# Optimization experiments

Measured on AMD Instinct MI355X. Metric: run time of the kernel, lower is better.

## Reference

```python
import jax, jax.numpy as jnp
import numpy as np

B, R, A, L, P = 1024, 512, 196, 2, 4  # batch, rnn_size, att_size, num_layers, num_parallels


def setup_inputs() -> dict:
    key = jax.random.key(0)
    ks = jax.random.split(key, 24)
    s = 0.02
    inp = {
        'x': jax.random.normal(ks[0], (B, R), jnp.float32),
        'att': jax.random.normal(ks[1], (B, A, R), jnp.float32),
        'inputs': jax.random.normal(ks[2], (2 * L, B, R), jnp.float32),
        # first attention block
        'Wa2a': jax.random.normal(ks[3], (A, R), jnp.float32) * s,
        'ba2a': jnp.zeros((A,), jnp.float32),
        'Wh2a': jax.random.normal(ks[4], (A, R), jnp.float32) * s,
        'bh2a': jnp.zeros((A,), jnp.float32),
        'Wd2d': jax.random.normal(ks[5], (1, A), jnp.float32) * s,
        'bd2d': jnp.zeros((1,), jnp.float32),
        # second attention block
        'Wa2a1': jax.random.normal(ks[6], (A, R), jnp.float32) * s,
        'ba2a1': jnp.zeros((A,), jnp.float32),
        'Wh2a1': jax.random.normal(ks[7], (A, R), jnp.float32) * s,
        'bh2a1': jnp.zeros((A,), jnp.float32),
        'Wd2d1': jax.random.normal(ks[8], (1, A), jnp.float32) * s,
        'bd2d1': jnp.zeros((1,), jnp.float32),
        # per-parallel LSTM gate linears, stacked over P
        'Wi2h': jax.random.normal(ks[9], (P, 4 * R, R), jnp.float32) * s,
        'bi2h': jnp.zeros((P, 4 * R), jnp.float32),
        'Wh2h': jax.random.normal(ks[10], (P, 4 * R, R), jnp.float32) * s,
        'bh2h': jnp.zeros((P, 4 * R), jnp.float32),
        'Wa2h': jax.random.normal(ks[11], (P, 4 * R, R), jnp.float32) * s,
        'ba2h': jnp.zeros((P, 4 * R), jnp.float32),
    }
    return inp


def _attend(att, h, Wa, ba, Wh, bh, Wd, bd):
    # att: [B, S, R] with S == A (code requires it); h: [B, R]
    av = jnp.einsum('bsr,ar->bsa', att, Wa) + ba            # [B, S, A]
    ah = h @ Wh.T + bh                                      # [B, A]
    # original expands h-projection along the LAST axis (unsqueeze(2).expand)
    dot = jnp.tanh(av + ah[:, :, None])                     # [B, S, A]
    score = jnp.einsum('bsa,a->bs', dot, Wd[0]) + bd[0]     # [B, S]
    w = jax.nn.softmax(score, axis=-1)
    return jnp.einsum('bsr,bs->br', att, w)                 # [B, R]


def reference(x, att, inputs, Wa2a, ba2a, Wh2a, bh2a, Wd2d, bd2d,
              Wa2a1, ba2a1, Wh2a1, bh2a1, Wd2d1, bd2d1,
              Wi2h, bi2h, Wh2h, bh2h, Wa2h, ba2h):
    R_ = x.shape[-1]
    L_ = inputs.shape[0] // 2
    outputs = []
    for i in range(L_):
        prev_c = inputs[2 * i]
        prev_h = inputs[2 * i + 1]
        xt = x if i == 0 else x + outputs[-1]
        att_res = _attend(att, prev_h, Wa2a, ba2a, Wh2a, bh2a, Wd2d, bd2d)
        # stacked per-parallel gate sums: [P, B, 4R]
        sums = (jnp.einsum('bd,pgd->pbg', xt, Wi2h) + bi2h[:, None, :]
                + jnp.einsum('bd,pgd->pbg', prev_h, Wh2h) + bh2h[:, None, :]
                + jnp.einsum('bd,pgd->pbg', att_res, Wa2h) + ba2h[:, None, :])
        ig = jax.nn.sigmoid(sums[..., :R_])
        fg = jax.nn.sigmoid(sums[..., R_:2 * R_])
        og = jax.nn.sigmoid(sums[..., 2 * R_:3 * R_])
        it = jnp.tanh(sums[..., 3 * R_:])
        nc = fg * prev_c[None] + ig * it                    # [P, B, R]
        next_c = nc.mean(axis=0)
        next_h = (og * jnp.tanh(nc)).mean(axis=0)
        att_res1 = _attend(att, next_h, Wa2a1, ba2a1, Wh2a1, bh2a1, Wd2d1, bd2d1)
        top_h = att_res1 + next_h
        outputs.append(next_c)
        outputs.append(top_h)
    return jnp.stack(outputs)  # [2L, B, R]
```

## Files before the change

### kernel.cpp

```cpp
#include <hip/hip_runtime.h>
#include <math.h>

typedef __attribute__((ext_vector_type(8))) unsigned short ushort8_t;
typedef __attribute__((ext_vector_type(8))) short bf16x8;
typedef __attribute__((ext_vector_type(4))) float f32x4;

namespace {

constexpr int Bn = 1024;
constexpr int Rn = 512;
constexpr int An = 196;
constexpr int Gn = 8192;
constexpr int Kcat = 1536;
constexpr int NP = 224;
constexpr long ROWS = (long)Bn * An;

__device__ __forceinline__ float b2f(unsigned short u) {
  union { unsigned int i; float f; } v; v.i = ((unsigned int)u) << 16; return v.f;
}
__device__ __forceinline__ unsigned short f2b(float f) {
  union { float f; unsigned int i; } v; v.f = f;
  unsigned int r = v.i + 0x7fffu + ((v.i >> 16) & 1u);
  return (unsigned short)(r >> 16);
}
__device__ __forceinline__ float sigmf(float x) {
  return __builtin_amdgcn_rcpf(1.f + __expf(-x));
}
__device__ __forceinline__ float tanhf_fast(float x) {
  const float e = __expf(2.f * x);
  return 1.f - 2.f * __builtin_amdgcn_rcpf(e + 1.f);
}

__global__ __launch_bounds__(256)
void f2b_copy(const float* __restrict__ src, unsigned short* __restrict__ dst, long n)
{
  long i = ((long)blockIdx.x * 256 + threadIdx.x) * 8;
  const long stride = (long)gridDim.x * 256 * 8;
  for (; i + 8 <= n; i += stride) {
    float4 a = *(const float4*)(src + i);
    float4 b = *(const float4*)(src + i + 4);
    ushort8_t o;
    o[0] = f2b(a.x); o[1] = f2b(a.y); o[2] = f2b(a.z); o[3] = f2b(a.w);
    o[4] = f2b(b.x); o[5] = f2b(b.y); o[6] = f2b(b.z); o[7] = f2b(b.w);
    *(ushort8_t*)(dst + i) = o;
  }
}

__global__ __launch_bounds__(256)
void pack_all(const float* __restrict__ Wa0, const float* __restrict__ Wa1,
              const float* __restrict__ Wh0, const float* __restrict__ Wh1,
              const float* __restrict__ inputs, const float* __restrict__ x,
              const float* __restrict__ Wi, const float* __restrict__ Wh,
              const float* __restrict__ Wa,
              unsigned short* __restrict__ Wp, unsigned short* __restrict__ whcat,
              unsigned short* __restrict__ h01,
              unsigned short* __restrict__ X20, unsigned short* __restrict__ X21,
              unsigned short* __restrict__ W2)
{
  const int blk = blockIdx.x;
  if (blk < 112) {
    long i = ((long)blk * 256 + threadIdx.x) * 8;
    if (i >= 2L * NP * 512) return;
    const int set = (int)(i / (NP * 512));
    const int rem = (int)(i % (NP * 512));
    const int row = rem / 512, k = rem % 512;
    ushort8_t o;
    if (row < An) {
      const float* s = (set ? Wa1 : Wa0) + (long)row * 512 + k;
      float4 a = *(const float4*)s, b = *(const float4*)(s + 4);
      o[0] = f2b(a.x); o[1] = f2b(a.y); o[2] = f2b(a.z); o[3] = f2b(a.w);
      o[4] = f2b(b.x); o[5] = f2b(b.y); o[6] = f2b(b.z); o[7] = f2b(b.w);
    } else {
      o = ushort8_t{0,0,0,0,0,0,0,0};
    }
    *(ushort8_t*)(Wp + i) = o;
  } else if (blk < 210) {
    long i = ((long)(blk - 112) * 256 + threadIdx.x) * 8;
    if (i >= 2L * An * 512) return;
    const long half = (long)An * 512;
    const float* s = (i < half) ? Wh0 + i : Wh1 + (i - half);
    float4 v0 = *(const float4*)s, v1 = *(const float4*)(s + 4);
    ushort8_t o;
    o[0] = f2b(v0.x); o[1] = f2b(v0.y); o[2] = f2b(v0.z); o[3] = f2b(v0.w);
    o[4] = f2b(v1.x); o[5] = f2b(v1.y); o[6] = f2b(v1.z); o[7] = f2b(v1.w);
    *(ushort8_t*)(whcat + i) = o;
  } else if (blk < 722) {
    long i = ((long)(blk - 210) * 256 + threadIdx.x) * 8;
    if (i >= 2L * Bn * 512) return;
    const long half = (long)Bn * 512;
    const float* s = (i < half) ? inputs + half + i : inputs + 3 * half + (i - half);
    float4 v0 = *(const float4*)s, v1 = *(const float4*)(s + 4);
    ushort8_t o;
    o[0] = f2b(v0.x); o[1] = f2b(v0.y); o[2] = f2b(v0.z); o[3] = f2b(v0.w);
    o[4] = f2b(v1.x); o[5] = f2b(v1.y); o[6] = f2b(v1.z); o[7] = f2b(v1.w);
    *(ushort8_t*)(h01 + i) = o;
  } else if (blk < 1490) {
    long i = ((long)(blk - 722) * 256 + threadIdx.x) * 8;
    if (i >= 3L * Bn * 512) return;
    const int sec = (int)(i / ((long)Bn * 512));
    const long r = i % ((long)Bn * 512);
    const int b = (int)(r >> 9);
    const int k = (int)(r & 511);
    const float* src = (sec == 0 ? x
                     : sec == 1 ? inputs + (long)Bn * Rn
                     : inputs + 3L * Bn * Rn) + r;
    unsigned short* dst = (sec == 2 ? X21 : X20) + (long)b * Kcat + (sec ? 512 : 0) + k;
    float4 v0 = *(const float4*)src, v1 = *(const float4*)(src + 4);
    ushort8_t o;
    o[0] = f2b(v0.x); o[1] = f2b(v0.y); o[2] = f2b(v0.z); o[3] = f2b(v0.w);
    o[4] = f2b(v1.x); o[5] = f2b(v1.y); o[6] = f2b(v1.z); o[7] = f2b(v1.w);
    *(ushort8_t*)dst = o;
  } else {
    long i = ((long)(blk - 1490) * 256 + threadIdx.x) * 8;
    if (i >= (long)Gn * Kcat) return;
    const int g = (int)(i / Kcat);
    const int k = (int)(i % Kcat);
    const float* src = (k < 512) ? Wi + (long)g * 512 + k
                     : (k < 1024) ? Wh + (long)g * 512 + (k - 512)
                     : Wa + (long)g * 512 + (k - 1024);
    float4 a = *(const float4*)src;
    float4 b = *(const float4*)(src + 4);
    ushort8_t o;
    o[0] = f2b(a.x); o[1] = f2b(a.y); o[2] = f2b(a.z); o[3] = f2b(a.w);
    o[4] = f2b(b.x); o[5] = f2b(b.y); o[6] = f2b(b.z); o[7] = f2b(b.w);
    *(ushort8_t*)(W2 + i) = o;
  }
}

__global__ __launch_bounds__(512, 4)
void av_cs(const unsigned short* __restrict__ A,
           const unsigned short* __restrict__ Wpad,
           const float* __restrict__ b0vec, const float* __restrict__ b1vec,
           const float* __restrict__ Wd,
           const float* __restrict__ ah0, const float* __restrict__ ah1,
           float* __restrict__ s0, float* __restrict__ s1,
           unsigned short* __restrict__ av_out)
{
  __shared__ unsigned short As[128 * 32];
  __shared__ unsigned short Bs[224 * 32];
  __shared__ float wds[NP], bas[NP];
  __shared__ float ahAs[128], ahBs[128];
  __shared__ float sbA[128], sbB[128];

  const int tid = threadIdx.x;
  const int lane = tid & 63, w = tid >> 6;
  const int wr = w >> 1, wc = w & 1;
  const int fr = lane & 15, q = lane >> 4;
  const int d = blockIdx.x;
  const int xt = ((d >> 4) << 3) | (d & 7);
  const int set = (d >> 3) & 1;
  const long row0 = (long)xt * 128;

  if (set == 0) {
    if (tid < NP) {
      wds[tid] = (tid < An) ? Wd[tid] : 0.f;
      bas[tid] = (tid < An) ? b0vec[tid] : 0.f;
    }
    if (tid >= 256 && tid < 384) ahAs[tid - 256] = ah0[row0 + tid - 256];
    if (tid >= 384)              ahBs[tid - 384] = ah1[row0 + tid - 384];
  } else {
    if (tid < NP) bas[tid] = (tid < An) ? b1vec[tid] : 0.f;
  }

  const unsigned short* Ab = A + row0 * 512;
  const unsigned short* Bb = Wpad + (long)set * NP * 512;

  f32x4 acc[2][7] = {};

  const int grow = lane >> 2;
  const int gchk = (lane & 3) * 8;

  for (int kt = 0; kt < 512; kt += 32) {
    {
      const unsigned short* src = Ab + (long)(w * 16 + grow) * 512 + gchk + kt;
      __builtin_amdgcn_global_load_lds(
          (const __attribute__((address_space(1))) unsigned int*)src,
          (__attribute__((address_space(3))) unsigned int*)(As + w * 512), 16, 0, 0);
    }
    {
      const unsigned short* src = Bb + (long)(w * 16 + grow) * 512 + gchk + kt;
      __builtin_amdgcn_global_load_lds(
          (const __attribute__((address_space(1))) unsigned int*)src,
          (__attribute__((address_space(3))) unsigned int*)(Bs + w * 512), 16, 0, 0);
    }
    if (w < 6) {
      const unsigned short* src = Bb + (long)((w + 8) * 16 + grow) * 512 + gchk + kt;
      __builtin_amdgcn_global_load_lds(
          (const __attribute__((address_space(1))) unsigned int*)src,
          (__attribute__((address_space(3))) unsigned int*)(Bs + (w + 8) * 512), 16, 0, 0);
    }
    __syncthreads();
    bf16x8 af[2], bfr[7];
#pragma unroll
    for (int m = 0; m < 2; ++m)
      af[m] = *(const bf16x8*)&As[(wr * 32 + m * 16 + fr) * 32 + q * 8];
#pragma unroll
    for (int n = 0; n < 7; ++n)
      bfr[n] = *(const bf16x8*)&Bs[(wc * 112 + n * 16 + fr) * 32 + q * 8];
#pragma unroll
    for (int m = 0; m < 2; ++m)
#pragma unroll
      for (int n = 0; n < 7; ++n)
        acc[m][n] = __builtin_amdgcn_mfma_f32_16x16x32_bf16(af[m], bfr[n], acc[m][n], 0, 0, 0);
    __syncthreads();
  }

  if (set == 0) {
    float pA[2][4], pB[2][4];
#pragma unroll
    for (int m = 0; m < 2; ++m)
#pragma unroll
      for (int j = 0; j < 4; ++j) { pA[m][j] = 0.f; pB[m][j] = 0.f; }
#pragma unroll
    for (int n = 0; n < 7; ++n) {
      const int col = wc * 112 + n * 16 + fr;
      const float wd = wds[col];
      const float bv = bas[col];
#pragma unroll
      for (int m = 0; m < 2; ++m) {
#pragma unroll
        for (int j = 0; j < 4; ++j) {
          const int rl = wr * 32 + m * 16 + q * 4 + j;
          const float av = acc[m][n][j] + bv;
          pA[m][j] += wd * tanhf_fast(av + ahAs[rl]);
          pB[m][j] += wd * tanhf_fast(av + ahBs[rl]);
        }
      }
    }
#pragma unroll
    for (int m = 0; m < 2; ++m)
#pragma unroll
      for (int j = 0; j < 4; ++j) {
#pragma unroll
        for (int off = 1; off < 16; off <<= 1) {
          pA[m][j] += __shfl_xor(pA[m][j], off);
          pB[m][j] += __shfl_xor(pB[m][j], off);
        }
      }
    __syncthreads();
    if (wc == 0 && fr == 0) {
#pragma unroll
      for (int m = 0; m < 2; ++m)
#pragma unroll
        for (int j = 0; j < 4; ++j) {
          const int rl = wr * 32 + m * 16 + q * 4 + j;
          sbA[rl] = pA[m][j]; sbB[rl] = pB[m][j];
        }
    }
    __syncthreads();
    if (wc == 1 && fr == 0) {
#pragma unroll
      for (int m = 0; m < 2; ++m)
#pragma unroll
        for (int j = 0; j < 4; ++j) {
          const int rl = wr * 32 + m * 16 + q * 4 + j;
          sbA[rl] += pA[m][j]; sbB[rl] += pB[m][j];
        }
    }
    __syncthreads();
    if (tid < 128) {
      s0[row0 + tid] = sbA[tid];
      s1[row0 + tid] = sbB[tid];
    }
  } else {
#pragma unroll
    for (int n = 0; n < 7; ++n) {
      const int col = wc * 112 + n * 16 + fr;
      if (col >= An) continue;
      const float bv = bas[col];
#pragma unroll
      for (int m = 0; m < 2; ++m) {
#pragma unroll
        for (int j = 0; j < 4; ++j) {
          const long row = row0 + wr * 32 + m * 16 + q * 4 + j;
          av_out[row * An + col] = f2b(acc[m][n][j] + bv);
        }
      }
    }
  }
}

__global__ __launch_bounds__(256)
void gemm_gate(const unsigned short* __restrict__ A, const unsigned short* __restrict__ Bm,
               const float* __restrict__ b1, const float* __restrict__ b2,
               const float* __restrict__ b3, float* __restrict__ C)
{
  __shared__ unsigned short As[128 * 32];
  __shared__ unsigned short Bs[128 * 32];
  const int tid = threadIdx.x;
  const int lane = tid & 63, w = tid >> 6;
  int bid = blockIdx.x;
  bid = (bid & 7) * (gridDim.x >> 3) + (bid >> 3);
  const int bx = bid & 63;
  const int by = bid >> 6;
  const long row0 = (long)by * 128;
  const long col0 = (long)bx * 128;
  const int wr = w >> 1, wc = w & 1;
  const int fr = lane & 15, q = lane >> 4;
  const int srow = lane >> 2, schk = lane & 3;

  f32x4 acc[4][4] = {};
  const unsigned short* A0 = A + row0 * Kcat + schk * 8;
  const unsigned short* B0 = Bm + col0 * Kcat + schk * 8;

  for (int kt = 0; kt < Kcat; kt += 32) {
#pragma unroll
    for (int i = 0; i < 2; ++i) {
      const int rr = (w * 2 + i) * 16 + srow;
      __builtin_amdgcn_global_load_lds(
          (const __attribute__((address_space(1))) unsigned int*)(A0 + (long)rr * Kcat + kt),
          (__attribute__((address_space(3))) unsigned int*)(As + (w * 2 + i) * 512),
          16, 0, 0);
      __builtin_amdgcn_global_load_lds(
          (const __attribute__((address_space(1))) unsigned int*)(B0 + (long)rr * Kcat + kt),
          (__attribute__((address_space(3))) unsigned int*)(Bs + (w * 2 + i) * 512),
          16, 0, 0);
    }
    __syncthreads();
    bf16x8 af[4], bfr[4];
#pragma unroll
    for (int m = 0; m < 4; ++m)
      af[m] = *(const bf16x8*)&As[(wr * 64 + m * 16 + fr) * 32 + q * 8];
#pragma unroll
    for (int n = 0; n < 4; ++n)
      bfr[n] = *(const bf16x8*)&Bs[(wc * 64 + n * 16 + fr) * 32 + q * 8];
#pragma unroll
    for (int m = 0; m < 4; ++m)
#pragma unroll
      for (int n = 0; n < 4; ++n)
        acc[m][n] = __builtin_amdgcn_mfma_f32_16x16x32_bf16(af[m], bfr[n], acc[m][n], 0, 0, 0);
    __syncthreads();
  }

  const int crow = wr * 64 + q * 4;
  const int ccol = wc * 64 + fr;
#pragma unroll
  for (int n = 0; n < 4; ++n) {
    const int col = (int)col0 + ccol + n * 16;
    const float bv = b1[col] + b2[col] + b3[col];
#pragma unroll
    for (int m = 0; m < 4; ++m) {
      const long rb = row0 + crow + m * 16;
#pragma unroll
      for (int j = 0; j < 4; ++j)
        C[(rb + j) * (long)Gn + col] = acc[m][n][j] + bv;
    }
  }
}

__global__ __launch_bounds__(256)
void gemm_bf(const unsigned short* __restrict__ A, const unsigned short* __restrict__ Bm,
             const float* __restrict__ bias, float* __restrict__ C,
             int N, int K, int ldc)
{
  constexpr int LDP = 56;
  __shared__ unsigned short As[128 * LDP];
  __shared__ unsigned short Bs[128 * LDP];
  const int tid = threadIdx.x;
  const long row0 = (long)blockIdx.y * 128;
  const int col0 = blockIdx.x * 128;
  const int wid = tid >> 6, lane = tid & 63;
  const int wr = wid >> 1, wc = wid & 1;
  const int fr = lane & 15, kg = (lane >> 4) * 8;

  f32x4 acc[4][4] = {};

  const int srow = tid >> 1;
  const int skh = tid & 1;
  const unsigned short* Ap = A + (row0 + srow) * (long)K + skh * 16;
  const int bcol = col0 + srow;
  const unsigned short* Bp = Bm + (long)(bcol < N ? bcol : N - 1) * K + skh * 16;

  ushort8_t a0 = *(const ushort8_t*)(Ap);
  ushort8_t a1 = *(const ushort8_t*)(Ap + 8);
  ushort8_t b0 = *(const ushort8_t*)(Bp);
  ushort8_t b1 = *(const ushort8_t*)(Bp + 8);

  const int sw = srow * LDP + skh * 16;
  for (int kt = 0; kt < K; kt += 32) {
    *(ushort8_t*)&As[sw] = a0;
    *(ushort8_t*)&As[sw + 8] = a1;
    *(ushort8_t*)&Bs[sw] = b0;
    *(ushort8_t*)&Bs[sw + 8] = b1;
    if (kt + 32 < K) {
      a0 = *(const ushort8_t*)(Ap + kt + 32);
      a1 = *(const ushort8_t*)(Ap + kt + 40);
      b0 = *(const ushort8_t*)(Bp + kt + 32);
      b1 = *(const ushort8_t*)(Bp + kt + 40);
    }
    __syncthreads();
    bf16x8 af[4], bfr[4];
#pragma unroll
    for (int m = 0; m < 4; ++m)
      af[m] = *(const bf16x8*)&As[(wr * 64 + m * 16 + fr) * LDP + kg];
#pragma unroll
    for (int n = 0; n < 4; ++n)
      bfr[n] = *(const bf16x8*)&Bs[(wc * 64 + n * 16 + fr) * LDP + kg];
#pragma unroll
    for (int m = 0; m < 4; ++m)
#pragma unroll
      for (int n = 0; n < 4; ++n)
        acc[m][n] = __builtin_amdgcn_mfma_f32_16x16x32_bf16(af[m], bfr[n], acc[m][n], 0, 0, 0);
    __syncthreads();
  }

  const int crow = wr * 64 + (lane >> 4) * 4;
  const int ccol = wc * 64 + fr;
#pragma unroll
  for (int n = 0; n < 4; ++n) {
    const int col = col0 + ccol + n * 16;
    if (col >= N) continue;
    const float bv = bias ? bias[col] : 0.f;
#pragma unroll
    for (int m = 0; m < 4; ++m) {
      const long rb = row0 + crow + m * 16;
#pragma unroll
      for (int j = 0; j < 4; ++j)
        C[(rb + j) * (long)ldc + col] = acc[m][n][j] + bv;
    }
  }
}

__global__ __launch_bounds__(256)
void score1(const unsigned short* __restrict__ av, const float* __restrict__ ah,
            const float* __restrict__ Wd, float* __restrict__ s0)
{
  const int row = blockIdx.x * 4 + (threadIdx.x >> 6);
  const int lane = threadIdx.x & 63;
  const float A0 = ah[row];
  float v0 = 0.f;
  if (lane < 49) {
    ushort4 u = *(const ushort4*)(av + (long)row * An + lane * 4);
    float4 w = *(const float4*)(Wd + lane * 4);
    v0 = w.x * tanhf_fast(b2f(u.x) + A0) + w.y * tanhf_fast(b2f(u.y) + A0)
       + w.z * tanhf_fast(b2f(u.z) + A0) + w.w * tanhf_fast(b2f(u.w) + A0);
  }
#pragma unroll
  for (int o = 32; o; o >>= 1) v0 += __shfl_down(v0, o);
  if (lane == 0) s0[row] = v0;
}

__global__ __launch_bounds__(256)
void wsumA(const unsigned short* __restrict__ att,
           const float* __restrict__ scA, const float* __restrict__ scB,
           unsigned short* __restrict__ X20, unsigned short* __restrict__ X21)
{
  const int half = threadIdx.x >> 7;
  const int b = blockIdx.x * 2 + half;
  const int t = threadIdx.x & 127;
  const int wv = t >> 6;
  __shared__ float ws0[2][An], ws1[2][An];
  __shared__ float redm[2][2][2], redsum[2][2][2];

  const float r0a = scA[(long)b * An + t];
  const float r0b = (t + 128 < An) ? scA[(long)b * An + t + 128] : -3.0e38f;
  const float r1a = scB[(long)b * An + t];
  const float r1b = (t + 128 < An) ? scB[(long)b * An + t + 128] : -3.0e38f;
  float m0 = fmaxf(r0a, r0b), m1 = fmaxf(r1a, r1b);
#pragma unroll
  for (int o = 32; o; o >>= 1) {
    m0 = fmaxf(m0, __shfl_xor(m0, o));
    m1 = fmaxf(m1, __shfl_xor(m1, o));
  }
  if ((t & 63) == 0) { redm[0][half][wv] = m0; redm[1][half][wv] = m1; }
  __syncthreads();
  m0 = fmaxf(redm[0][half][0], redm[0][half][1]);
  m1 = fmaxf(redm[1][half][0], redm[1][half][1]);
  const float e0a = __expf(r0a - m0);
  const float e0b = (t + 128 < An) ? __expf(r0b - m0) : 0.f;
  const float e1a = __expf(r1a - m1);
  const float e1b = (t + 128 < An) ? __expf(r1b - m1) : 0.f;
  float sl0 = e0a + e0b, sl1 = e1a + e1b;
#pragma unroll
  for (int o = 32; o; o >>= 1) {
    sl0 += __shfl_xor(sl0, o);
    sl1 += __shfl_xor(sl1, o);
  }
  if ((t & 63) == 0) { redsum[0][half][wv] = sl0; redsum[1][half][wv] = sl1; }
  __syncthreads();
  const float inv0 = __builtin_amdgcn_rcpf(redsum[0][half][0] + redsum[0][half][1]);
  const float inv1 = __builtin_amdgcn_rcpf(redsum[1][half][0] + redsum[1][half][1]);
  ws0[half][t] = e0a * inv0;
  ws1[half][t] = e1a * inv1;
  if (t + 128 < An) {
    ws0[half][t + 128] = e0b * inv0;
    ws1[half][t + 128] = e1b * inv1;
  }
  __syncthreads();

  const unsigned short* ap = att + (long)b * An * Rn + t * 4;
  float a00 = 0, a01 = 0, a02 = 0, a03 = 0;
  float a10 = 0, a11 = 0, a12 = 0, a13 = 0;
  for (int s = 0; s < An; ++s) {
    ushort4 u = *(const ushort4*)(ap + (long)s * Rn);
    const float f0 = b2f(u.x), f1 = b2f(u.y), f2 = b2f(u.z), f3 = b2f(u.w);
    const float v0 = ws0[half][s];
    a00 = fmaf(f0, v0, a00); a01 = fmaf(f1, v0, a01);
    a02 = fmaf(f2, v0, a02); a03 = fmaf(f3, v0, a03);
    const float v1 = ws1[half][s];
    a10 = fmaf(f0, v1, a10); a11 = fmaf(f1, v1, a11);
    a12 = fmaf(f2, v1, a12); a13 = fmaf(f3, v1, a13);
  }
  const long base = (long)b * Kcat + 1024 + t * 4;
  ushort4 oA, oB;
  oA.x = f2b(a00); oA.y = f2b(a01); oA.z = f2b(a02); oA.w = f2b(a03);
  oB.x = f2b(a10); oB.y = f2b(a11); oB.z = f2b(a12); oB.w = f2b(a13);
  *(ushort4*)(X20 + base) = oA;
  *(ushort4*)(X21 + base) = oB;
}

template<bool WX2>
__global__ __launch_bounds__(256)
void wsumB(const unsigned short* __restrict__ att,
           const float* __restrict__ sc, const float* __restrict__ nh,
           const float* __restrict__ xin,
           float* __restrict__ outp, unsigned short* __restrict__ X21)
{
  const int half = threadIdx.x >> 7;
  const int b = blockIdx.x * 2 + half;
  const int t = threadIdx.x & 127;
  const int wv = t >> 6;
  __shared__ float ws[2][An];
  __shared__ float redm[2][2], redsum[2][2];

  const float ra = sc[(long)b * An + t];
  const float rb = (t + 128 < An) ? sc[(long)b * An + t + 128] : -3.0e38f;
  float m0 = fmaxf(ra, rb);
#pragma unroll
  for (int o = 32; o; o >>= 1) m0 = fmaxf(m0, __shfl_xor(m0, o));
  if ((t & 63) == 0) redm[half][wv] = m0;
  __syncthreads();
  m0 = fmaxf(redm[half][0], redm[half][1]);
  const float ea = __expf(ra - m0);
  const float eb = (t + 128 < An) ? __expf(rb - m0) : 0.f;
  float sl = ea + eb;
#pragma unroll
  for (int o = 32; o; o >>= 1) sl += __shfl_xor(sl, o);
  if ((t & 63) == 0) redsum[half][wv] = sl;
  __syncthreads();
  const float inv = __builtin_amdgcn_rcpf(redsum[half][0] + redsum[half][1]);
  ws[half][t] = ea * inv;
  if (t + 128 < An) ws[half][t + 128] = eb * inv;
  __syncthreads();

  const unsigned short* ap = att + (long)b * An * Rn + t * 4;
  float a0 = 0, a1 = 0, a2 = 0, a3 = 0;
  for (int s = 0; s < An; ++s) {
    ushort4 u = *(const ushort4*)(ap + (long)s * Rn);
    const float w = ws[half][s];
    a0 = fmaf(b2f(u.x), w, a0); a1 = fmaf(b2f(u.y), w, a1);
    a2 = fmaf(b2f(u.z), w, a2); a3 = fmaf(b2f(u.w), w, a3);
  }
  const long base = (long)b * Rn + t * 4;
  float4 ad = *(const float4*)(nh + base);
  a0 += ad.x; a1 += ad.y; a2 += ad.z; a3 += ad.w;
  *(float4*)(outp + base) = make_float4(a0, a1, a2, a3);
  if (WX2) {
    float4 xv = *(const float4*)(xin + base);
    ushort4 o;
    o.x = f2b(a0 + xv.x); o.y = f2b(a1 + xv.y);
    o.z = f2b(a2 + xv.z); o.w = f2b(a3 + xv.w);
    *(ushort4*)(X21 + (long)b * Kcat + t * 4) = o;
  }
}

__global__ __launch_bounds__(256)
void gates_pw(const float* __restrict__ sums, const float* __restrict__ prev_c,
              float* __restrict__ out_c, float* __restrict__ nh,
              unsigned short* __restrict__ nh_bf)
{
  const int i = blockIdx.x * 256 + threadIdx.x;
  const int b = i >> 9;
  const int r = i & 511;
  const float c = prev_c[i];
  float aC = 0.f, aH = 0.f;
#pragma unroll
  for (int p = 0; p < 4; ++p) {
    const float* sp = sums + (long)b * Gn + p * 2048 + r;
    const float ig = sigmf(sp[0]);
    const float fg = sigmf(sp[512]);
    const float og = sigmf(sp[1024]);
    const float it = tanhf_fast(sp[1536]);
    const float nc = fmaf(fg, c, ig * it);
    aC += nc;
    aH = fmaf(og, tanhf_fast(nc), aH);
  }
  out_c[i] = aC * 0.25f;
  const float hv = aH * 0.25f;
  nh[i] = hv;
  nh_bf[i] = f2b(hv);
}

}

extern "C" void kernel_launch(void* const* d_in, const int* in_sizes, int n_in,
                              void* d_out, int out_size, void* d_ws, size_t ws_size,
                              hipStream_t stream)
{
  const float* x      = (const float*)d_in[0];
  const float* att    = (const float*)d_in[1];
  const float* inputs = (const float*)d_in[2];
  const float* Wa2a   = (const float*)d_in[3];
  const float* ba2a   = (const float*)d_in[4];
  const float* Wh2a   = (const float*)d_in[5];
  const float* bh2a   = (const float*)d_in[6];
  const float* Wd2d   = (const float*)d_in[7];
  const float* Wa2a1  = (const float*)d_in[9];
  const float* ba2a1  = (const float*)d_in[10];
  const float* Wh2a1  = (const float*)d_in[11];
  const float* bh2a1  = (const float*)d_in[12];
  const float* Wd2d1  = (const float*)d_in[13];
  const float* Wi2h   = (const float*)d_in[15];
  const float* bi2h   = (const float*)d_in[16];
  const float* Wh2h   = (const float*)d_in[17];
  const float* bh2h   = (const float*)d_in[18];
  const float* Wa2h   = (const float*)d_in[19];
  const float* ba2h   = (const float*)d_in[20];
  (void)in_sizes; (void)n_in; (void)out_size; (void)ws_size;

  float* out = (float*)d_out;
  const float* prev_c0 = inputs + 0 * (long)Bn * Rn;
  const float* prev_c1 = inputs + 2 * (long)Bn * Rn;

  char* wsp = (char*)d_ws;
  size_t off = 0;
  auto alloc = [&](size_t bytes) -> void* {
    void* p = wsp + off;
    off += (bytes + 1023) & ~(size_t)1023;
    return p;
  };
  unsigned short* att_bf  = (unsigned short*)alloc(ROWS * Rn * 2);
  unsigned short* W2      = (unsigned short*)alloc((size_t)Gn * Kcat * 2);
  unsigned short* Wpad    = (unsigned short*)alloc((size_t)2 * NP * Rn * 2);
  unsigned short* whcat   = (unsigned short*)alloc((size_t)2 * An * Rn * 2);
  unsigned short* h01_bf  = (unsigned short*)alloc((size_t)2 * Bn * Rn * 2);
  unsigned short* nh_bf   = (unsigned short*)alloc((size_t)Bn * Rn * 2);
  unsigned short* X20     = (unsigned short*)alloc((size_t)Bn * Kcat * 2);
  unsigned short* X21     = (unsigned short*)alloc((size_t)Bn * Kcat * 2);
  unsigned short* av1_bf  = (unsigned short*)alloc(ROWS * An * 2);
  float* ahAB = (float*)alloc((size_t)2 * ROWS * 4);
  float* ah1  = (float*)alloc(ROWS * 4);
  float* scA  = (float*)alloc(ROWS * 4);
  float* scB  = (float*)alloc(ROWS * 4);
  float* sc1  = (float*)alloc(ROWS * 4);
  float* nh   = (float*)alloc((size_t)Bn * Rn * 4);
  float* sums = (float*)alloc((size_t)Bn * Gn * 4);

  float* ahA = ahAB;
  float* ahB = ahAB + ROWS;
  unsigned short* wh2a_bf  = whcat;
  unsigned short* wh2a1_bf = whcat + (size_t)An * Rn;

  const dim3 blk(256);

  f2b_copy<<<dim3(50176), blk, 0, stream>>>(att, att_bf, ROWS * Rn);
  pack_all<<<dim3(7634), blk, 0, stream>>>(Wa2a, Wa2a1, Wh2a, Wh2a1, inputs, x,
                                           Wi2h, Wh2h, Wa2h,
                                           Wpad, whcat, h01_bf, X20, X21, W2);

  gemm_bf<<<dim3(2, 16), blk, 0, stream>>>(h01_bf, wh2a_bf, bh2a, ahA, An, Rn, An);

  av_cs<<<dim3(3136), dim3(512), 0, stream>>>(
      att_bf, Wpad, ba2a, ba2a1, Wd2d, ahA, ahB, scA, scB, av1_bf);

  wsumA<<<dim3(Bn / 2), blk, 0, stream>>>(att_bf, scA, scB, X20, X21);

  gemm_gate<<<dim3(512), blk, 0, stream>>>(X20, W2, bi2h, bh2h, ba2h, sums);
  gates_pw<<<dim3(Bn * Rn / 256), blk, 0, stream>>>(sums, prev_c0, out + 0, nh, nh_bf);

  gemm_bf<<<dim3(2, Bn / 128), blk, 0, stream>>>(nh_bf, wh2a1_bf, bh2a1, ah1, An, Rn, An);
  score1<<<dim3((int)(ROWS / 4)), blk, 0, stream>>>(av1_bf, ah1, Wd2d1, sc1);
  wsumB<true><<<dim3(Bn / 2), blk, 0, stream>>>(att_bf, sc1, nh, x,
                                                out + (long)Bn * Rn, X21);

  gemm_gate<<<dim3(512), blk, 0, stream>>>(X21, W2, bi2h, bh2h, ba2h, sums);
  gates_pw<<<dim3(Bn * Rn / 256), blk, 0, stream>>>(sums, prev_c1, out + 2 * (long)Bn * Rn, nh, nh_bf);

  gemm_bf<<<dim3(2, Bn / 128), blk, 0, stream>>>(nh_bf, wh2a1_bf, bh2a1, ah1, An, Rn, An);
  score1<<<dim3((int)(ROWS / 4)), blk, 0, stream>>>(av1_bf, ah1, Wd2d1, sc1);
  wsumB<false><<<dim3(Bn / 2), blk, 0, stream>>>(att_bf, sc1, nh, (const float*)nullptr,
                                                 out + 3 * (long)Bn * Rn,
                                                 (unsigned short*)nullptr);
}
```

Baseline: 659.0 us.

## Double K-tile with XOR swizzle in av_cs; fuse ah1 projection into score kernel

The av_cs GEMM now loads 64-wide K tiles into LDS using an XOR-swizzled column layout. This halves the number of barrier-separated iterations and cuts LDS bank conflicts on fragment reads. Separately, the small ah1 = nh @ Wh2a1^T GEMM is removed and computed inside the score kernel as a per-row wave dot product. That saves two launches and the ah1 buffer, but each (b,s) row now recomputes a 512-length dot product that reads nh and Wh rows from cache, which adds redundant arithmetic and memory traffic.

```diff
diff --git a/kernel.cpp b/kernel.cpp
--- a/kernel.cpp
+++ b/kernel.cpp
@@ -136,8 +136,8 @@
            float* __restrict__ s0, float* __restrict__ s1,
            unsigned short* __restrict__ av_out)
 {
-  __shared__ unsigned short As[128 * 32];
-  __shared__ unsigned short Bs[224 * 32];
+  __shared__ unsigned short As[128 * 64];
+  __shared__ unsigned short Bs[224 * 64];
   __shared__ float wds[NP], bas[NP];
   __shared__ float ahAs[128], ahBs[128];
   __shared__ float sbA[128], sbB[128];
@@ -167,41 +167,60 @@
 
   f32x4 acc[2][7] = {};
 
-  const int grow = lane >> 2;
-  const int gchk = (lane & 3) * 8;
-
-  for (int kt = 0; kt < 512; kt += 32) {
-    {
-      const unsigned short* src = Ab + (long)(w * 16 + grow) * 512 + gchk + kt;
+  const int lr = lane >> 3;
+  const int lc = (lane & 7) ^ lr;
+
+  for (int kt = 0; kt < 512; kt += 64) {
+#pragma unroll
+    for (int i = 0; i < 2; ++i) {
+      const int r = w * 16 + i * 8 + lr;
+      const unsigned short* src = Ab + (long)r * 512 + kt + lc * 8;
       __builtin_amdgcn_global_load_lds(
           (const __attribute__((address_space(1))) unsigned int*)src,
-          (__attribute__((address_space(3))) unsigned int*)(As + w * 512), 16, 0, 0);
-    }
-    {
-      const unsigned short* src = Bb + (long)(w * 16 + grow) * 512 + gchk + kt;
+          (__attribute__((address_space(3))) unsigned int*)(As + (w * 16 + i * 8) * 64),
+          16, 0, 0);
+    }
+#pragma unroll
+    for (int i = 0; i < 3; ++i) {
+      const int g = w + i * 8;
+      const int r = g * 8 + lr;
+      const unsigned short* src = Bb + (long)r * 512 + kt + lc * 8;
       __builtin_amdgcn_global_load_lds(
           (const __attribute__((address_space(1))) unsigned int*)src,
-          (__attribute__((address_space(3))) unsigned int*)(Bs + w * 512), 16, 0, 0);
-    }
-    if (w < 6) {
-      const unsigned short* src = Bb + (long)((w + 8) * 16 + grow) * 512 + gchk + kt;
+          (__attribute__((address_space(3))) unsigned int*)(Bs + g * 8 * 64),
+          16, 0, 0);
+    }
+    if (w < 4) {
+      const int g = w + 24;
+      const int r = g * 8 + lr;
+      const unsigned short* src = Bb + (long)r * 512 + kt + lc * 8;
       __builtin_amdgcn_global_load_lds(
           (const __attribute__((address_space(1))) unsigned int*)src,
-          (__attribute__((address_space(3))) unsigned int*)(Bs + (w + 8) * 512), 16, 0, 0);
-    }
-    __syncthreads();
-    bf16x8 af[2], bfr[7];
-#pragma unroll
-    for (int m = 0; m < 2; ++m)
-      af[m] = *(const bf16x8*)&As[(wr * 32 + m * 16 + fr) * 32 + q * 8];
-#pragma unroll
-    for (int n = 0; n < 7; ++n)
-      bfr[n] = *(const bf16x8*)&Bs[(wc * 112 + n * 16 + fr) * 32 + q * 8];
-#pragma unroll
-    for (int m = 0; m < 2; ++m)
-#pragma unroll
-      for (int n = 0; n < 7; ++n)
-        acc[m][n] = __builtin_amdgcn_mfma_f32_16x16x32_bf16(af[m], bfr[n], acc[m][n], 0, 0, 0);
+          (__attribute__((address_space(3))) unsigned int*)(Bs + g * 8 * 64),
+          16, 0, 0);
+    }
+    __syncthreads();
+#pragma unroll
+    for (int s = 0; s < 2; ++s) {
+      bf16x8 af[2], bfr[7];
+#pragma unroll
+      for (int m = 0; m < 2; ++m) {
+        const int ar = wr * 32 + m * 16 + fr;
+        const int cp = (s * 4 + q) ^ (ar & 7);
+        af[m] = *(const bf16x8*)&As[ar * 64 + cp * 8];
+      }
+#pragma unroll
+      for (int n = 0; n < 7; ++n) {
+        const int br = wc * 112 + n * 16 + fr;
+        const int cp = (s * 4 + q) ^ (br & 7);
+        bfr[n] = *(const bf16x8*)&Bs[br * 64 + cp * 8];
+      }
+#pragma unroll
+      for (int m = 0; m < 2; ++m)
+#pragma unroll
+        for (int n = 0; n < 7; ++n)
+          acc[m][n] = __builtin_amdgcn_mfma_f32_16x16x32_bf16(af[m], bfr[n], acc[m][n], 0, 0, 0);
+    }
     __syncthreads();
   }
 
@@ -422,12 +441,28 @@
 }
 
 __global__ __launch_bounds__(256)
-void score1(const unsigned short* __restrict__ av, const float* __restrict__ ah,
-            const float* __restrict__ Wd, float* __restrict__ s0)
+void score1f(const unsigned short* __restrict__ av,
+             const unsigned short* __restrict__ nh_bf,
+             const unsigned short* __restrict__ wh1,
+             const float* __restrict__ bh1,
+             const float* __restrict__ Wd, float* __restrict__ s0)
 {
   const int row = blockIdx.x * 4 + (threadIdx.x >> 6);
   const int lane = threadIdx.x & 63;
-  const float A0 = ah[row];
+  const int b = row / An;
+  const int s = row - b * An;
+
+  float dot = 0.f;
+  {
+    ushort8_t nv = *(const ushort8_t*)(nh_bf + (long)b * 512 + lane * 8);
+    ushort8_t wv = *(const ushort8_t*)(wh1 + (long)s * 512 + lane * 8);
+#pragma unroll
+    for (int j = 0; j < 8; ++j) dot = fmaf(b2f(nv[j]), b2f(wv[j]), dot);
+  }
+#pragma unroll
+  for (int o = 32; o; o >>= 1) dot += __shfl_xor(dot, o);
+  const float A0 = dot + bh1[s];
+
   float v0 = 0.f;
   if (lane < 49) {
     ushort4 u = *(const ushort4*)(av + (long)row * An + lane * 4);
@@ -639,7 +674,6 @@
   unsigned short* X21     = (unsigned short*)alloc((size_t)Bn * Kcat * 2);
   unsigned short* av1_bf  = (unsigned short*)alloc(ROWS * An * 2);
   float* ahAB = (float*)alloc((size_t)2 * ROWS * 4);
-  float* ah1  = (float*)alloc(ROWS * 4);
   float* scA  = (float*)alloc(ROWS * 4);
   float* scB  = (float*)alloc(ROWS * 4);
   float* sc1  = (float*)alloc(ROWS * 4);
@@ -668,16 +702,14 @@
   gemm_gate<<<dim3(512), blk, 0, stream>>>(X20, W2, bi2h, bh2h, ba2h, sums);
   gates_pw<<<dim3(Bn * Rn / 256), blk, 0, stream>>>(sums, prev_c0, out + 0, nh, nh_bf);
 
-  gemm_bf<<<dim3(2, Bn / 128), blk, 0, stream>>>(nh_bf, wh2a1_bf, bh2a1, ah1, An, Rn, An);
-  score1<<<dim3((int)(ROWS / 4)), blk, 0, stream>>>(av1_bf, ah1, Wd2d1, sc1);
+  score1f<<<dim3((int)(ROWS / 4)), blk, 0, stream>>>(av1_bf, nh_bf, wh2a1_bf, bh2a1, Wd2d1, sc1);
   wsumB<true><<<dim3(Bn / 2), blk, 0, stream>>>(att_bf, sc1, nh, x,
                                                 out + (long)Bn * Rn, X21);
 
   gemm_gate<<<dim3(512), blk, 0, stream>>>(X21, W2, bi2h, bh2h, ba2h, sums);
   gates_pw<<<dim3(Bn * Rn / 256), blk, 0, stream>>>(sums, prev_c1, out + 2 * (long)Bn * Rn, nh, nh_bf);
 
-  gemm_bf<<<dim3(2, Bn / 128), blk, 0, stream>>>(nh_bf, wh2a1_bf, bh2a1, ah1, An, Rn, An);
-  score1<<<dim3((int)(ROWS / 4)), blk, 0, stream>>>(av1_bf, ah1, Wd2d1, sc1);
+  score1f<<<dim3((int)(ROWS / 4)), blk, 0, stream>>>(av1_bf, nh_bf, wh2a1_bf, bh2a1, Wd2d1, sc1);
   wsumB<false><<<dim3(Bn / 2), blk, 0, stream>>>(att_bf, sc1, nh, (const float*)nullptr,
                                                  out + 3 * (long)Bn * Rn,
                                                  (unsigned short*)nullptr);
```

New measurement: 729.9 us. 10.8% more time.
